# Kernel optimization log

Measured on AMD Instinct MI355X. Metric: run time of the kernel, lower is better.

The kernel has to match this reference:

```python
import jax, jax.numpy as jnp
import numpy as np

B, S, D_MODEL, N_HEADS, HEAD_DIM = 4, 2048, 1024, 16, 64
NEG = -1e9


def apply_rope_real(x, cos_f, sin_f):
    # x: [B, H, S, D]; cos_f/sin_f: [S, D//2] broadcast over B, H
    x_even = x[..., ::2]
    x_odd = x[..., 1::2]
    out_even = x_even * cos_f - x_odd * sin_f
    out_odd = x_even * sin_f + x_odd * cos_f
    return jnp.stack([out_even, out_odd], axis=-1).reshape(x.shape)


def setup_inputs() -> dict:
    key = jax.random.key(0)
    ks = jax.random.split(key, 8)
    x = jax.random.normal(ks[0], (B, S, D_MODEL), dtype=jnp.float32)
    # RoPE tables: theta_i = 10000^{-2i/d}, angles = pos * theta
    inv_freq = 1.0 / (10000.0 ** (jnp.arange(0, HEAD_DIM, 2, dtype=jnp.float32) / HEAD_DIM))
    angles = jnp.arange(S, dtype=jnp.float32)[:, None] * inv_freq[None, :]  # [S, D/2]
    cos_freqs = jnp.cos(angles)
    sin_freqs = jnp.sin(angles)
    causal_mask = jnp.where(jnp.tril(jnp.ones((S, S), dtype=bool)), 0.0, NEG).astype(jnp.float32)
    scale = 0.02
    w_q = jax.random.normal(ks[1], (D_MODEL, D_MODEL), dtype=jnp.float32) * scale
    w_k = jax.random.normal(ks[2], (D_MODEL, D_MODEL), dtype=jnp.float32) * scale
    w_v = jax.random.normal(ks[3], (D_MODEL, D_MODEL), dtype=jnp.float32) * scale
    w_o = jax.random.normal(ks[4], (D_MODEL, D_MODEL), dtype=jnp.float32) * scale
    return {"x": x, "cos_freqs": cos_freqs, "sin_freqs": sin_freqs,
            "causal_mask": causal_mask, "w_q": w_q, "w_k": w_k, "w_v": w_v, "w_o": w_o}


def reference(x, cos_freqs, sin_freqs, causal_mask, w_q, w_k, w_v, w_o):
    batch, seq_len, _ = x.shape
    scale = 1.0 / jnp.sqrt(jnp.float32(HEAD_DIM))
    # torch Linear: y = x @ W.T
    def proj(w):
        return (x @ w.T).reshape(batch, seq_len, N_HEADS, HEAD_DIM).transpose(0, 2, 1, 3)
    q = apply_rope_real(proj(w_q), cos_freqs, sin_freqs)
    k = apply_rope_real(proj(w_k), cos_freqs, sin_freqs)
    v = proj(w_v)
    attn = jnp.einsum('bhqd,bhkd->bhqk', q, k) * scale + causal_mask
    attn = jax.nn.softmax(attn, axis=-1)
    out = jnp.einsum('bhqk,bhkd->bhqd', attn, v)
    out = out.transpose(0, 2, 1, 3).reshape(batch, seq_len, -1)
    return out @ w_o.T
```

## Files before the change

kernel.cpp:

```cpp
#include <hip/hip_runtime.h>
#include <stdint.h>

#define B_  4
#define S_  2048
#define DM_ 1024
#define NH_ 16
#define HD_ 64

typedef unsigned short ushort_t;
typedef __bf16 bf16x8 __attribute__((ext_vector_type(8)));
typedef float  floatx4 __attribute__((ext_vector_type(4)));
typedef float  floatx16 __attribute__((ext_vector_type(16)));

__device__ __forceinline__ float bf2f(ushort_t u) {
    union { unsigned int i; float f; } v; v.i = ((unsigned int)u) << 16; return v.f;
}
__device__ __forceinline__ ushort_t f2bf(float f) {
    union { float f; unsigned int i; } v; v.f = f;
    unsigned int x = v.i;
    return (ushort_t)((x + 0x7fffu + ((x >> 16) & 1u)) >> 16);
}
__device__ __forceinline__ unsigned int pack_bf16_trunc(float lo, float hi) {
    union { float f; unsigned int u; } a, b;
    a.f = lo; b.f = hi;
    return __builtin_amdgcn_perm(b.u, a.u, 0x07060302u);
}

__global__ __launch_bounds__(256) void cvt_all_kernel(
    const float* __restrict__ x,  const float* __restrict__ wq,
    const float* __restrict__ wk, const float* __restrict__ wv,
    const float* __restrict__ wo,
    ushort_t* __restrict__ xb,  ushort_t* __restrict__ wqb,
    ushort_t* __restrict__ wkb, ushort_t* __restrict__ wvb,
    ushort_t* __restrict__ wob)
{
    const int blk = blockIdx.x;
    const float* src; ushort_t* dst; int off;
    if (blk < 8192)       { src = x;  dst = xb;  off = blk; }
    else if (blk < 9216)  { src = wq; dst = wqb; off = blk - 8192; }
    else if (blk < 10240) { src = wk; dst = wkb; off = blk - 9216; }
    else if (blk < 11264) { src = wv; dst = wvb; off = blk - 10240; }
    else                  { src = wo; dst = wob; off = blk - 11264; }
    const int i = off * 256 + threadIdx.x;
    float4 v = ((const float4*)src)[i];
    ushort4 o; o.x = f2bf(v.x); o.y = f2bf(v.y); o.z = f2bf(v.z); o.w = f2bf(v.w);
    ((ushort4*)dst)[i] = o;
}

__global__ __launch_bounds__(512, 2) void gemm_bt_kernel(
    const ushort_t* __restrict__ A,
    const ushort_t* __restrict__ B0, const ushort_t* __restrict__ B1,
    const ushort_t* __restrict__ B2,
    void* __restrict__ C0, void* __restrict__ C1, void* __restrict__ C2,
    int M, int N, int K, int mode, int nz)
{
    __shared__ ushort_t As[2][16384];
    __shared__ ushort_t Bs[2][8192];

    const int lid = blockIdx.x;
    const int cpx = gridDim.x >> 3;
    const int wg  = (lid & 7) * cpx + (lid >> 3);
    const int x   = wg / (8 * nz);
    const int rr  = wg - x * (8 * nz);
    const int y   = rr & 7;
    const int z   = rr >> 3;

    const ushort_t* Bw = z == 0 ? B0 : z == 1 ? B1 : B2;
    void* Cv           = z == 0 ? C0 : z == 1 ? C1 : C2;

    const int tid  = threadIdx.x;
    const int wave = tid >> 6, lane = tid & 63;
    const int l15 = lane & 15, quad = lane >> 4;
    const int wr = wave >> 1, wc = wave & 1;
    const int mbase = x * 256;
    const int nbase = y * 128;
    const int NT = K >> 6;

    auto stageA = [&](int bt, int t, int L0) {
#pragma unroll
        for (int L = L0; L < L0 + 2; ++L) {
            const int e8  = L * 512 + tid;
            const int row = e8 >> 3, c = e8 & 7;
            const ushort_t* src = A + (size_t)(mbase + row) * K + t * 64 + ((c ^ (row & 7)) << 3);
            __builtin_amdgcn_global_load_lds(
                (const __attribute__((address_space(1))) unsigned int*)src,
                (__attribute__((address_space(3))) unsigned int*)(&As[bt][e8 * 8]), 16, 0, 0);
        }
    };
    auto stageB = [&](int bt, int t, int L) {
        const int e8  = L * 512 + tid;
        const int row = e8 >> 3, c = e8 & 7;
        const ushort_t* src = Bw + (size_t)(nbase + row) * K + t * 64 + ((c ^ (row & 7)) << 3);
        __builtin_amdgcn_global_load_lds(
            (const __attribute__((address_space(1))) unsigned int*)src,
            (__attribute__((address_space(3))) unsigned int*)(&Bs[bt][e8 * 8]), 16, 0, 0);
    };

    floatx4 acc[4][4] = {};

    stageA(0, 0, 0); stageA(0, 0, 2);
    stageB(0, 0, 0); stageB(0, 0, 1);
    if (NT > 1) {
        stageB(1, 1, 0); stageB(1, 1, 1);
        asm volatile("s_waitcnt vmcnt(2)" ::: "memory");
    } else {
        asm volatile("s_waitcnt vmcnt(0)" ::: "memory");
    }
    __builtin_amdgcn_s_barrier();

    auto do_tile = [&](int t, int bt) {
        bf16x8 a0[2][2], a1[2][2], b0[2][2], b1[2][2];
#pragma unroll
        for (int kk = 0; kk < 2; ++kk) {
#pragma unroll
            for (int f = 0; f < 2; ++f) {
                const int row = wr * 64 + f * 16 + l15;
                a0[kk][f] = *(const bf16x8*)&As[bt][row * 64 + ((((kk << 2) | quad)) ^ (l15 & 7)) * 8];
            }
#pragma unroll
            for (int g = 0; g < 2; ++g) {
                const int row = wc * 64 + g * 16 + l15;
                b0[kk][g] = *(const bf16x8*)&Bs[bt][row * 64 + ((((kk << 2) | quad)) ^ (l15 & 7)) * 8];
            }
        }
        if (t + 1 < NT) stageA(bt ^ 1, t + 1, 0);
        __builtin_amdgcn_s_barrier();
        asm volatile("s_waitcnt lgkmcnt(0)" ::: "memory");
        __builtin_amdgcn_s_setprio(1);
#pragma unroll
        for (int kk = 0; kk < 2; ++kk)
#pragma unroll
            for (int mt = 0; mt < 2; ++mt)
#pragma unroll
                for (int nt = 0; nt < 2; ++nt)
                    acc[mt][nt] = __builtin_amdgcn_mfma_f32_16x16x32_bf16(
                        a0[kk][mt], b0[kk][nt], acc[mt][nt], 0, 0, 0);
        __builtin_amdgcn_s_setprio(0);
        __builtin_amdgcn_s_barrier();

#pragma unroll
        for (int kk = 0; kk < 2; ++kk)
#pragma unroll
            for (int g = 0; g < 2; ++g) {
                const int row = wc * 64 + 32 + g * 16 + l15;
                b1[kk][g] = *(const bf16x8*)&Bs[bt][row * 64 + ((((kk << 2) | quad)) ^ (l15 & 7)) * 8];
            }
        if (t + 1 < NT) stageA(bt ^ 1, t + 1, 2);
        __builtin_amdgcn_s_barrier();
        asm volatile("s_waitcnt lgkmcnt(0)" ::: "memory");
        __builtin_amdgcn_s_setprio(1);
#pragma unroll
        for (int kk = 0; kk < 2; ++kk)
#pragma unroll
            for (int mt = 0; mt < 2; ++mt)
#pragma unroll
                for (int nt = 0; nt < 2; ++nt)
                    acc[mt][2 + nt] = __builtin_amdgcn_mfma_f32_16x16x32_bf16(
                        a0[kk][mt], b1[kk][nt], acc[mt][2 + nt], 0, 0, 0);
        __builtin_amdgcn_s_setprio(0);
        __builtin_amdgcn_s_barrier();

#pragma unroll
        for (int kk = 0; kk < 2; ++kk)
#pragma unroll
            for (int f = 0; f < 2; ++f) {
                const int row = wr * 64 + 32 + f * 16 + l15;
                a1[kk][f] = *(const bf16x8*)&As[bt][row * 64 + ((((kk << 2) | quad)) ^ (l15 & 7)) * 8];
            }
        if (t + 2 < NT) stageB(bt, t + 2, 0);
        __builtin_amdgcn_s_barrier();
        asm volatile("s_waitcnt lgkmcnt(0)" ::: "memory");
        __builtin_amdgcn_s_setprio(1);
#pragma unroll
        for (int kk = 0; kk < 2; ++kk)
#pragma unroll
            for (int mt = 0; mt < 2; ++mt)
#pragma unroll
                for (int nt = 0; nt < 2; ++nt)
                    acc[2 + mt][2 + nt] = __builtin_amdgcn_mfma_f32_16x16x32_bf16(
                        a1[kk][mt], b1[kk][nt], acc[2 + mt][2 + nt], 0, 0, 0);
        __builtin_amdgcn_s_setprio(0);
        __builtin_amdgcn_s_barrier();

        if (t + 2 < NT) stageB(bt, t + 2, 1);
        __builtin_amdgcn_s_barrier();
        __builtin_amdgcn_s_setprio(1);
#pragma unroll
        for (int kk = 0; kk < 2; ++kk)
#pragma unroll
            for (int mt = 0; mt < 2; ++mt)
#pragma unroll
                for (int nt = 0; nt < 2; ++nt)
                    acc[2 + mt][nt] = __builtin_amdgcn_mfma_f32_16x16x32_bf16(
                        a1[kk][mt], b0[kk][nt], acc[2 + mt][nt], 0, 0, 0);
        __builtin_amdgcn_s_setprio(0);
        if (t + 2 < NT) { asm volatile("s_waitcnt vmcnt(2)" ::: "memory"); }
        else            { asm volatile("s_waitcnt vmcnt(0)" ::: "memory"); }
        __builtin_amdgcn_s_barrier();
    };

    for (int t = 0; t < NT; t += 2) {
        do_tile(t, 0);
        do_tile(t + 1, 1);
    }

    const bool vtmode = (mode == 0) && (z == 2);
#pragma unroll
    for (int mt = 0; mt < 4; ++mt) {
#pragma unroll
        for (int nt = 0; nt < 4; ++nt) {
            const int col = nbase + wc * 64 + nt * 16 + l15;
            const int m0  = mbase + wr * 64 + mt * 16 + quad * 4;
            if (vtmode) {
                const int b = m0 >> 11, s = m0 & 2047;
                const int hh = col >> 6, d = col & 63;
                uint2 pk;
                pk.x = (unsigned)f2bf(acc[mt][nt][0]) | ((unsigned)f2bf(acc[mt][nt][1]) << 16);
                pk.y = (unsigned)f2bf(acc[mt][nt][2]) | ((unsigned)f2bf(acc[mt][nt][3]) << 16);
                *(uint2*)&((ushort_t*)Cv)[((size_t)((b * NH_ + hh) * HD_ + d)) * S_ + s] = pk;
            } else if (mode == 0) {
#pragma unroll
                for (int r = 0; r < 4; ++r) {
                    const int m = m0 + r;
                    const int b = m >> 11, s = m & 2047;
                    const int hh = col >> 6, d = col & 63;
                    ((ushort_t*)Cv)[(((size_t)(b * NH_ + hh)) * S_ + s) * HD_ + d] =
                        f2bf(acc[mt][nt][r]);
                }
            } else {
#pragma unroll
                for (int r = 0; r < 4; ++r)
                    ((float*)Cv)[(size_t)(m0 + r) * N + col] = acc[mt][nt][r];
            }
        }
    }
}

#define QSCALE 0.1803368801f
__global__ __launch_bounds__(256) void rope_kernel(
    ushort_t* __restrict__ q, ushort_t* __restrict__ k,
    const float* __restrict__ cf, const float* __restrict__ sf)
{
    const int idx = blockIdx.x * 256 + threadIdx.x;
    const int j = idx & 31;
    const int s = (idx >> 5) & (S_ - 1);
    const float c  = cf[s * 32 + j];
    const float sn = sf[s * 32 + j];
    const size_t base = (size_t)idx * 2;
    float qe = bf2f(q[base]), qo = bf2f(q[base + 1]);
    q[base]     = f2bf((qe * c - qo * sn) * QSCALE);
    q[base + 1] = f2bf((qe * sn + qo * c) * QSCALE);
    float ke = bf2f(k[base]), ko = bf2f(k[base + 1]);
    k[base]     = f2bf(ke * c - ko * sn);
    k[base + 1] = f2bf(ke * sn + ko * c);
}

__global__ __launch_bounds__(256, 2) void attn_kernel(
    const ushort_t* __restrict__ Qg, const ushort_t* __restrict__ Kg,
    const ushort_t* __restrict__ Vg, ushort_t* __restrict__ Og)
{
    __shared__ ushort_t Ks[2][64 * 64];
    __shared__ ushort_t Vt[2][64 * 64];
    __shared__ ushort_t Pt[4][32 * 64];

    const int pair = blockIdx.x;
    const int bh   = blockIdx.y;
    const int tid  = threadIdx.x;
    const int wave = tid >> 6, lane = tid & 63;
    const int l31 = lane & 31, h = lane >> 5;

    const size_t bh_off = (size_t)bh * S_ * HD_;
    const int pswz = (l31 & 7) << 3;
    const int b_out = bh >> 4, h_out = bh & 15;

    const int e0 = tid, e1 = tid + 256;
    const int r0 = e0 >> 3, c0 = (e0 & 7) ^ (r0 & 7);
    const int r1 = e1 >> 3, c1 = (e1 & 7) ^ (r1 & 7);

#pragma unroll 1
    for (int seg = 0; seg < 2; ++seg) {
        const int qtile = seg ? (15 - pair) : pair;
        const int qbase = qtile * 128;
        const int nkt   = 2 * qtile + 2;
        const int qrow  = qbase + wave * 32 + l31;

        bf16x8 qf[4];
#pragma unroll
        for (int ks = 0; ks < 4; ++ks)
            qf[ks] = *(const bf16x8*)(Qg + bh_off + (size_t)qrow * HD_ + ks * 16 + h * 8);

        float m_run = -1e30f, l_run = 0.f;
        floatx16 o_acc[2] = {};

        {
            const ushort_t* ka = Kg + bh_off + (size_t)r0 * HD_ + c0 * 8;
            const ushort_t* kb = Kg + bh_off + (size_t)r1 * HD_ + c1 * 8;
            const ushort_t* va = Vg + bh_off + (size_t)r0 * S_ + c0 * 8;
            const ushort_t* vb = Vg + bh_off + (size_t)r1 * S_ + c1 * 8;
            __builtin_amdgcn_global_load_lds(
                (const __attribute__((address_space(1))) unsigned int*)ka,
                (__attribute__((address_space(3))) unsigned int*)(&Ks[0][e0 * 8]), 16, 0, 0);
            __builtin_amdgcn_global_load_lds(
                (const __attribute__((address_space(1))) unsigned int*)kb,
                (__attribute__((address_space(3))) unsigned int*)(&Ks[0][e1 * 8]), 16, 0, 0);
            __builtin_amdgcn_global_load_lds(
                (const __attribute__((address_space(1))) unsigned int*)va,
                (__attribute__((address_space(3))) unsigned int*)(&Vt[0][e0 * 8]), 16, 0, 0);
            __builtin_amdgcn_global_load_lds(
                (const __attribute__((address_space(1))) unsigned int*)vb,
                (__attribute__((address_space(3))) unsigned int*)(&Vt[0][e1 * 8]), 16, 0, 0);
        }
        asm volatile("s_waitcnt vmcnt(0)" ::: "memory");
        __syncthreads();

        for (int kt = 0; kt < nkt; ++kt) {
            const int kbase = kt * 64;
            const int cur = kt & 1;

            if (kt + 1 < nkt) {
                const int nb = kbase + 64;
                const ushort_t* ka = Kg + bh_off + (size_t)(nb + r0) * HD_ + c0 * 8;
                const ushort_t* kb = Kg + bh_off + (size_t)(nb + r1) * HD_ + c1 * 8;
                const ushort_t* va = Vg + bh_off + (size_t)r0 * S_ + nb + c0 * 8;
                const ushort_t* vb = Vg + bh_off + (size_t)r1 * S_ + nb + c1 * 8;
                __builtin_amdgcn_global_load_lds(
                    (const __attribute__((address_space(1))) unsigned int*)ka,
                    (__attribute__((address_space(3))) unsigned int*)(&Ks[cur ^ 1][e0 * 8]), 16, 0, 0);
                __builtin_amdgcn_global_load_lds(
                    (const __attribute__((address_space(1))) unsigned int*)kb,
                    (__attribute__((address_space(3))) unsigned int*)(&Ks[cur ^ 1][e1 * 8]), 16, 0, 0);
                __builtin_amdgcn_global_load_lds(
                    (const __attribute__((address_space(1))) unsigned int*)va,
                    (__attribute__((address_space(3))) unsigned int*)(&Vt[cur ^ 1][e0 * 8]), 16, 0, 0);
                __builtin_amdgcn_global_load_lds(
                    (const __attribute__((address_space(1))) unsigned int*)vb,
                    (__attribute__((address_space(3))) unsigned int*)(&Vt[cur ^ 1][e1 * 8]), 16, 0, 0);
            }

            if (kbase <= qbase + wave * 32 + 31) {
                floatx16 st[2] = {};
#pragma unroll
                for (int nt = 0; nt < 2; ++nt) {
                    const int krow = nt * 32 + l31;
#pragma unroll
                    for (int ks = 0; ks < 4; ++ks) {
                        bf16x8 kf = *(const bf16x8*)&Ks[cur][krow * 64 +
                                        (((ks * 2 + h) ^ (l31 & 7)) << 3)];
                        st[nt] = __builtin_amdgcn_mfma_f32_32x32x16_bf16(kf, qf[ks], st[nt], 0, 0, 0);
                    }
                }
                if (kbase + 63 > qbase + wave * 32) {
#pragma unroll
                    for (int nt = 0; nt < 2; ++nt) {
                        const int key0 = kbase + nt * 32 + 4 * h;
#pragma unroll
                        for (int c = 0; c < 4; ++c)
#pragma unroll
                            for (int r = 0; r < 4; ++r)
                                if (key0 + 8 * c + r > qrow) st[nt][c * 4 + r] = -1e9f;
                    }
                }
                float mx = st[0][0];
#pragma unroll
                for (int nt = 0; nt < 2; ++nt)
#pragma unroll
                    for (int i = 0; i < 16; ++i) mx = fmaxf(mx, st[nt][i]);
                mx = fmaxf(mx, __shfl_xor(mx, 32, 64));
                const float mnew = fmaxf(m_run, mx);
                const float alpha = __builtin_amdgcn_exp2f(m_run - mnew);
                m_run = mnew;
                float sum = 0.f;
#pragma unroll
                for (int nt = 0; nt < 2; ++nt)
#pragma unroll
                    for (int i = 0; i < 16; ++i) {
                        const float p = __builtin_amdgcn_exp2f(st[nt][i] - mnew);
                        st[nt][i] = p; sum += p;
                    }
                sum += __shfl_xor(sum, 32, 64);
                l_run = l_run * alpha + sum;
#pragma unroll
                for (int dt = 0; dt < 2; ++dt)
#pragma unroll
                    for (int i = 0; i < 16; ++i) o_acc[dt][i] *= alpha;

                ushort_t* pr = &Pt[wave][l31 * 64];
#pragma unroll
                for (int nt = 0; nt < 2; ++nt)
#pragma unroll
                    for (int c = 0; c < 4; ++c) {
                        uint2 pk;
                        pk.x = pack_bf16_trunc(st[nt][c * 4 + 0], st[nt][c * 4 + 1]);
                        pk.y = pack_bf16_trunc(st[nt][c * 4 + 2], st[nt][c * 4 + 3]);
                        *(uint2*)(pr + (((nt * 32 + 8 * c) ^ pswz) + 4 * h)) = pk;
                    }
                __builtin_amdgcn_fence(__ATOMIC_ACQ_REL, "wavefront");
                __builtin_amdgcn_wave_barrier();

                bf16x8 pf[4];
#pragma unroll
                for (int ks = 0; ks < 4; ++ks)
                    pf[ks] = *(const bf16x8*)(&Pt[wave][l31 * 64 + ((ks * 16 + h * 8) ^ pswz)]);

#pragma unroll
                for (int dt = 0; dt < 2; ++dt) {
                    const int d = dt * 32 + l31;
#pragma unroll
                    for (int ks = 0; ks < 4; ++ks) {
                        bf16x8 vf = *(const bf16x8*)&Vt[cur][d * 64 +
                                        (((ks * 2 + h) ^ (l31 & 7)) << 3)];
                        o_acc[dt] = __builtin_amdgcn_mfma_f32_32x32x16_bf16(vf, pf[ks], o_acc[dt], 0, 0, 0);
                    }
                }
            }

            asm volatile("s_waitcnt vmcnt(0)" ::: "memory");
            __syncthreads();
        }

        const float inv = 1.0f / l_run;
        ushort_t* orow = Og + ((size_t)(b_out * S_ + qrow)) * DM_ + h_out * HD_;
#pragma unroll
        for (int dt = 0; dt < 2; ++dt)
#pragma unroll
            for (int c = 0; c < 4; ++c) {
                uint2 pk;
                pk.x = (unsigned)f2bf(o_acc[dt][c * 4 + 0] * inv) |
                       ((unsigned)f2bf(o_acc[dt][c * 4 + 1] * inv) << 16);
                pk.y = (unsigned)f2bf(o_acc[dt][c * 4 + 2] * inv) |
                       ((unsigned)f2bf(o_acc[dt][c * 4 + 3] * inv) << 16);
                *(uint2*)(orow + dt * 32 + 8 * c + 4 * h) = pk;
            }
    }
}

extern "C" void kernel_launch(void* const* d_in, const int* in_sizes, int n_in,
                              void* d_out, int out_size, void* d_ws, size_t ws_size,
                              hipStream_t stream)
{
    const float* x  = (const float*)d_in[0];
    const float* cf = (const float*)d_in[1];
    const float* sf = (const float*)d_in[2];
    const float* wq = (const float*)d_in[4];
    const float* wk = (const float*)d_in[5];
    const float* wv = (const float*)d_in[6];
    const float* wo = (const float*)d_in[7];
    float* out = (float*)d_out;

    const size_t NELEM = (size_t)B_ * S_ * DM_;
    const size_t WELEM = (size_t)DM_ * DM_;
    ushort_t* xb  = (ushort_t*)d_ws;
    ushort_t* qb  = xb + NELEM;
    ushort_t* kb  = qb + NELEM;
    ushort_t* vb  = kb + NELEM;
    ushort_t* ao  = vb + NELEM;
    ushort_t* wqb = ao + NELEM;
    ushort_t* wkb = wqb + WELEM;
    ushort_t* wvb = wkb + WELEM;
    ushort_t* wob = wvb + WELEM;

    cvt_all_kernel<<<dim3(8192 + 4 * 1024), 256, 0, stream>>>(
        x, wq, wk, wv, wo, xb, wqb, wkb, wvb, wob);

    const int M = B_ * S_;
    gemm_bt_kernel<<<dim3(32 * 8 * 3), 512, 0, stream>>>(
        xb, wqb, wkb, wvb, qb, kb, vb, M, DM_, DM_, 0, 3);
    rope_kernel<<<dim3((B_ * NH_ * S_ * 32) / 256), 256, 0, stream>>>(qb, kb, cf, sf);
    attn_kernel<<<dim3(8, B_ * NH_), 256, 0, stream>>>(qb, kb, vb, ao);
    gemm_bt_kernel<<<dim3(32 * 8), 512, 0, stream>>>(
        ao, wob, wob, wob, out, out, out, M, DM_, DM_, 1, 1);
}
```

Baseline: 285.8 us.

## Rework attention scheduling, keep P in registers via permlane swap, lazy rescale

Each attention block now handles a single q-tile instead of a pair, with 1024 blocks ordered longest-first and batch-heads interleaved across the grid. Occupancy rises to four blocks per CU. The P matrix is no longer staged through LDS; it is repacked in registers with permlane32_swap, which removes the Pt buffer and a wave barrier. Online-softmax rescaling is skipped unless the running max grows by more than a threshold, trading some exp range headroom for fewer multiplies.

```diff
diff --git a/kernel.cpp b/kernel.cpp
--- a/kernel.cpp
+++ b/kernel.cpp
@@ -255,183 +255,185 @@
     k[base + 1] = f2bf(ke * sn + ko * c);
 }
 
-__global__ __launch_bounds__(256, 2) void attn_kernel(
+__global__ __launch_bounds__(256, 4) void attn_kernel(
     const ushort_t* __restrict__ Qg, const ushort_t* __restrict__ Kg,
     const ushort_t* __restrict__ Vg, ushort_t* __restrict__ Og)
 {
     __shared__ ushort_t Ks[2][64 * 64];
     __shared__ ushort_t Vt[2][64 * 64];
-    __shared__ ushort_t Pt[4][32 * 64];
-
-    const int pair = blockIdx.x;
-    const int bh   = blockIdx.y;
+
+    const int id   = blockIdx.x;
+    const int sg   = id >> 3;
+    const int bh   = (id & 7) * 8 + (sg & 7);
+    const int qtile = 15 - (sg >> 3);
     const int tid  = threadIdx.x;
     const int wave = tid >> 6, lane = tid & 63;
     const int l31 = lane & 31, h = lane >> 5;
 
     const size_t bh_off = (size_t)bh * S_ * HD_;
-    const int pswz = (l31 & 7) << 3;
     const int b_out = bh >> 4, h_out = bh & 15;
 
     const int e0 = tid, e1 = tid + 256;
     const int r0 = e0 >> 3, c0 = (e0 & 7) ^ (r0 & 7);
     const int r1 = e1 >> 3, c1 = (e1 & 7) ^ (r1 & 7);
 
-#pragma unroll 1
-    for (int seg = 0; seg < 2; ++seg) {
-        const int qtile = seg ? (15 - pair) : pair;
-        const int qbase = qtile * 128;
-        const int nkt   = 2 * qtile + 2;
-        const int qrow  = qbase + wave * 32 + l31;
-
-        bf16x8 qf[4];
-#pragma unroll
-        for (int ks = 0; ks < 4; ++ks)
-            qf[ks] = *(const bf16x8*)(Qg + bh_off + (size_t)qrow * HD_ + ks * 16 + h * 8);
-
-        float m_run = -1e30f, l_run = 0.f;
-        floatx16 o_acc[2] = {};
-
-        {
-            const ushort_t* ka = Kg + bh_off + (size_t)r0 * HD_ + c0 * 8;
-            const ushort_t* kb = Kg + bh_off + (size_t)r1 * HD_ + c1 * 8;
-            const ushort_t* va = Vg + bh_off + (size_t)r0 * S_ + c0 * 8;
-            const ushort_t* vb = Vg + bh_off + (size_t)r1 * S_ + c1 * 8;
+    const int qbase = qtile * 128;
+    const int nkt   = 2 * qtile + 2;
+    const int qrow  = qbase + wave * 32 + l31;
+
+    bf16x8 qf[4];
+#pragma unroll
+    for (int ks = 0; ks < 4; ++ks)
+        qf[ks] = *(const bf16x8*)(Qg + bh_off + (size_t)qrow * HD_ + ks * 16 + h * 8);
+
+    float m_run = -1e30f, l_run = 0.f;
+    floatx16 o_acc[2] = {};
+
+    {
+        const ushort_t* ka = Kg + bh_off + (size_t)r0 * HD_ + c0 * 8;
+        const ushort_t* kb = Kg + bh_off + (size_t)r1 * HD_ + c1 * 8;
+        const ushort_t* va = Vg + bh_off + (size_t)r0 * S_ + c0 * 8;
+        const ushort_t* vb = Vg + bh_off + (size_t)r1 * S_ + c1 * 8;
+        __builtin_amdgcn_global_load_lds(
+            (const __attribute__((address_space(1))) unsigned int*)ka,
+            (__attribute__((address_space(3))) unsigned int*)(&Ks[0][e0 * 8]), 16, 0, 0);
+        __builtin_amdgcn_global_load_lds(
+            (const __attribute__((address_space(1))) unsigned int*)kb,
+            (__attribute__((address_space(3))) unsigned int*)(&Ks[0][e1 * 8]), 16, 0, 0);
+        __builtin_amdgcn_global_load_lds(
+            (const __attribute__((address_space(1))) unsigned int*)va,
+            (__attribute__((address_space(3))) unsigned int*)(&Vt[0][e0 * 8]), 16, 0, 0);
+        __builtin_amdgcn_global_load_lds(
+            (const __attribute__((address_space(1))) unsigned int*)vb,
+            (__attribute__((address_space(3))) unsigned int*)(&Vt[0][e1 * 8]), 16, 0, 0);
+    }
+    asm volatile("s_waitcnt vmcnt(0)" ::: "memory");
+    __syncthreads();
+
+    for (int kt = 0; kt < nkt; ++kt) {
+        const int kbase = kt * 64;
+        const int cur = kt & 1;
+
+        if (kt + 1 < nkt) {
+            const int nb = kbase + 64;
+            const ushort_t* ka = Kg + bh_off + (size_t)(nb + r0) * HD_ + c0 * 8;
+            const ushort_t* kb = Kg + bh_off + (size_t)(nb + r1) * HD_ + c1 * 8;
+            const ushort_t* va = Vg + bh_off + (size_t)r0 * S_ + nb + c0 * 8;
+            const ushort_t* vb = Vg + bh_off + (size_t)r1 * S_ + nb + c1 * 8;
             __builtin_amdgcn_global_load_lds(
                 (const __attribute__((address_space(1))) unsigned int*)ka,
-                (__attribute__((address_space(3))) unsigned int*)(&Ks[0][e0 * 8]), 16, 0, 0);
+                (__attribute__((address_space(3))) unsigned int*)(&Ks[cur ^ 1][e0 * 8]), 16, 0, 0);
             __builtin_amdgcn_global_load_lds(
                 (const __attribute__((address_space(1))) unsigned int*)kb,
-                (__attribute__((address_space(3))) unsigned int*)(&Ks[0][e1 * 8]), 16, 0, 0);
+                (__attribute__((address_space(3))) unsigned int*)(&Ks[cur ^ 1][e1 * 8]), 16, 0, 0);
             __builtin_amdgcn_global_load_lds(
                 (const __attribute__((address_space(1))) unsigned int*)va,
-                (__attribute__((address_space(3))) unsigned int*)(&Vt[0][e0 * 8]), 16, 0, 0);
+                (__attribute__((address_space(3))) unsigned int*)(&Vt[cur ^ 1][e0 * 8]), 16, 0, 0);
             __builtin_amdgcn_global_load_lds(
                 (const __attribute__((address_space(1))) unsigned int*)vb,
-                (__attribute__((address_space(3))) unsigned int*)(&Vt[0][e1 * 8]), 16, 0, 0);
-        }
-        asm volatile("s_waitcnt vmcnt(0)" ::: "memory");
-        __syncthreads();
-
-        for (int kt = 0; kt < nkt; ++kt) {
-            const int kbase = kt * 64;
-            const int cur = kt & 1;
-
-            if (kt + 1 < nkt) {
-                const int nb = kbase + 64;
-                const ushort_t* ka = Kg + bh_off + (size_t)(nb + r0) * HD_ + c0 * 8;
-                const ushort_t* kb = Kg + bh_off + (size_t)(nb + r1) * HD_ + c1 * 8;
-                const ushort_t* va = Vg + bh_off + (size_t)r0 * S_ + nb + c0 * 8;
-                const ushort_t* vb = Vg + bh_off + (size_t)r1 * S_ + nb + c1 * 8;
-                __builtin_amdgcn_global_load_lds(
-                    (const __attribute__((address_space(1))) unsigned int*)ka,
-                    (__attribute__((address_space(3))) unsigned int*)(&Ks[cur ^ 1][e0 * 8]), 16, 0, 0);
-                __builtin_amdgcn_global_load_lds(
-                    (const __attribute__((address_space(1))) unsigned int*)kb,
-                    (__attribute__((address_space(3))) unsigned int*)(&Ks[cur ^ 1][e1 * 8]), 16, 0, 0);
-                __builtin_amdgcn_global_load_lds(
-                    (const __attribute__((address_space(1))) unsigned int*)va,
-                    (__attribute__((address_space(3))) unsigned int*)(&Vt[cur ^ 1][e0 * 8]), 16, 0, 0);
-                __builtin_amdgcn_global_load_lds(
-                    (const __attribute__((address_space(1))) unsigned int*)vb,
-                    (__attribute__((address_space(3))) unsigned int*)(&Vt[cur ^ 1][e1 * 8]), 16, 0, 0);
-            }
-
-            if (kbase <= qbase + wave * 32 + 31) {
-                floatx16 st[2] = {};
+                (__attribute__((address_space(3))) unsigned int*)(&Vt[cur ^ 1][e1 * 8]), 16, 0, 0);
+        }
+
+        if (kbase <= qbase + wave * 32 + 31) {
+            floatx16 st[2] = {};
+#pragma unroll
+            for (int nt = 0; nt < 2; ++nt) {
+                const int krow = nt * 32 + l31;
+#pragma unroll
+                for (int ks = 0; ks < 4; ++ks) {
+                    bf16x8 kf = *(const bf16x8*)&Ks[cur][krow * 64 +
+                                    (((ks * 2 + h) ^ (l31 & 7)) << 3)];
+                    st[nt] = __builtin_amdgcn_mfma_f32_32x32x16_bf16(kf, qf[ks], st[nt], 0, 0, 0);
+                }
+            }
+            if (kbase + 63 > qbase + wave * 32) {
 #pragma unroll
                 for (int nt = 0; nt < 2; ++nt) {
-                    const int krow = nt * 32 + l31;
-#pragma unroll
-                    for (int ks = 0; ks < 4; ++ks) {
-                        bf16x8 kf = *(const bf16x8*)&Ks[cur][krow * 64 +
-                                        (((ks * 2 + h) ^ (l31 & 7)) << 3)];
-                        st[nt] = __builtin_amdgcn_mfma_f32_32x32x16_bf16(kf, qf[ks], st[nt], 0, 0, 0);
-                    }
-                }
-                if (kbase + 63 > qbase + wave * 32) {
-#pragma unroll
-                    for (int nt = 0; nt < 2; ++nt) {
-                        const int key0 = kbase + nt * 32 + 4 * h;
-#pragma unroll
-                        for (int c = 0; c < 4; ++c)
-#pragma unroll
-                            for (int r = 0; r < 4; ++r)
-                                if (key0 + 8 * c + r > qrow) st[nt][c * 4 + r] = -1e9f;
-                    }
-                }
-                float mx = st[0][0];
-#pragma unroll
-                for (int nt = 0; nt < 2; ++nt)
-#pragma unroll
-                    for (int i = 0; i < 16; ++i) mx = fmaxf(mx, st[nt][i]);
-                mx = fmaxf(mx, __shfl_xor(mx, 32, 64));
+                    const int key0 = kbase + nt * 32 + 4 * h;
+#pragma unroll
+                    for (int c = 0; c < 4; ++c)
+#pragma unroll
+                        for (int r = 0; r < 4; ++r)
+                            if (key0 + 8 * c + r > qrow) st[nt][c * 4 + r] = -1e9f;
+                }
+            }
+            float mx = st[0][0];
+#pragma unroll
+            for (int nt = 0; nt < 2; ++nt)
+#pragma unroll
+                for (int i = 0; i < 16; ++i) mx = fmaxf(mx, st[nt][i]);
+            mx = fmaxf(mx, __shfl_xor(mx, 32, 64));
+            if (!__all(mx <= m_run + 8.0f)) {
                 const float mnew = fmaxf(m_run, mx);
                 const float alpha = __builtin_amdgcn_exp2f(m_run - mnew);
                 m_run = mnew;
-                float sum = 0.f;
-#pragma unroll
-                for (int nt = 0; nt < 2; ++nt)
-#pragma unroll
-                    for (int i = 0; i < 16; ++i) {
-                        const float p = __builtin_amdgcn_exp2f(st[nt][i] - mnew);
-                        st[nt][i] = p; sum += p;
-                    }
-                sum += __shfl_xor(sum, 32, 64);
-                l_run = l_run * alpha + sum;
+                l_run *= alpha;
 #pragma unroll
                 for (int dt = 0; dt < 2; ++dt)
 #pragma unroll
                     for (int i = 0; i < 16; ++i) o_acc[dt][i] *= alpha;
-
-                ushort_t* pr = &Pt[wave][l31 * 64];
-#pragma unroll
-                for (int nt = 0; nt < 2; ++nt)
-#pragma unroll
-                    for (int c = 0; c < 4; ++c) {
-                        uint2 pk;
-                        pk.x = pack_bf16_trunc(st[nt][c * 4 + 0], st[nt][c * 4 + 1]);
-                        pk.y = pack_bf16_trunc(st[nt][c * 4 + 2], st[nt][c * 4 + 3]);
-                        *(uint2*)(pr + (((nt * 32 + 8 * c) ^ pswz) + 4 * h)) = pk;
-                    }
-                __builtin_amdgcn_fence(__ATOMIC_ACQ_REL, "wavefront");
-                __builtin_amdgcn_wave_barrier();
-
-                bf16x8 pf[4];
-#pragma unroll
-                for (int ks = 0; ks < 4; ++ks)
-                    pf[ks] = *(const bf16x8*)(&Pt[wave][l31 * 64 + ((ks * 16 + h * 8) ^ pswz)]);
-
-#pragma unroll
-                for (int dt = 0; dt < 2; ++dt) {
-                    const int d = dt * 32 + l31;
-#pragma unroll
-                    for (int ks = 0; ks < 4; ++ks) {
-                        bf16x8 vf = *(const bf16x8*)&Vt[cur][d * 64 +
-                                        (((ks * 2 + h) ^ (l31 & 7)) << 3)];
-                        o_acc[dt] = __builtin_amdgcn_mfma_f32_32x32x16_bf16(vf, pf[ks], o_acc[dt], 0, 0, 0);
-                    }
-                }
-            }
-
-            asm volatile("s_waitcnt vmcnt(0)" ::: "memory");
-            __syncthreads();
-        }
-
-        const float inv = 1.0f / l_run;
-        ushort_t* orow = Og + ((size_t)(b_out * S_ + qrow)) * DM_ + h_out * HD_;
-#pragma unroll
-        for (int dt = 0; dt < 2; ++dt)
-#pragma unroll
-            for (int c = 0; c < 4; ++c) {
-                uint2 pk;
-                pk.x = (unsigned)f2bf(o_acc[dt][c * 4 + 0] * inv) |
-                       ((unsigned)f2bf(o_acc[dt][c * 4 + 1] * inv) << 16);
-                pk.y = (unsigned)f2bf(o_acc[dt][c * 4 + 2] * inv) |
-                       ((unsigned)f2bf(o_acc[dt][c * 4 + 3] * inv) << 16);
-                *(uint2*)(orow + dt * 32 + 8 * c + 4 * h) = pk;
-            }
+            }
+            float sum = 0.f;
+#pragma unroll
+            for (int nt = 0; nt < 2; ++nt)
+#pragma unroll
+                for (int i = 0; i < 16; ++i) {
+                    const float p = __builtin_amdgcn_exp2f(st[nt][i] - m_run);
+                    st[nt][i] = p; sum += p;
+                }
+            sum += __shfl_xor(sum, 32, 64);
+            l_run += sum;
+
+            bf16x8 pf[4];
+#pragma unroll
+            for (int ks = 0; ks < 4; ++ks) {
+                const int nt = ks >> 1, base = (ks & 1) * 8;
+                unsigned wrd[4];
+#pragma unroll
+                for (int d8 = 0; d8 < 2; ++d8) {
+                    unsigned p = pack_bf16_trunc(st[nt][base + 2 * d8],
+                                                 st[nt][base + 2 * d8 + 1]);
+                    unsigned q = pack_bf16_trunc(st[nt][base + 4 + 2 * d8],
+                                                 st[nt][base + 4 + 2 * d8 + 1]);
+                    auto r = __builtin_amdgcn_permlane32_swap((int)p, (int)q, false, false);
+                    wrd[d8]     = (unsigned)r[0];
+                    wrd[2 + d8] = (unsigned)r[1];
+                }
+                union { unsigned u[4]; bf16x8 v; } cvt;
+                cvt.u[0] = wrd[0]; cvt.u[1] = wrd[1];
+                cvt.u[2] = wrd[2]; cvt.u[3] = wrd[3];
+                pf[ks] = cvt.v;
+            }
+
+#pragma unroll
+            for (int dt = 0; dt < 2; ++dt) {
+                const int d = dt * 32 + l31;
+#pragma unroll
+                for (int ks = 0; ks < 4; ++ks) {
+                    bf16x8 vf = *(const bf16x8*)&Vt[cur][d * 64 +
+                                    (((ks * 2 + h) ^ (l31 & 7)) << 3)];
+                    o_acc[dt] = __builtin_amdgcn_mfma_f32_32x32x16_bf16(vf, pf[ks], o_acc[dt], 0, 0, 0);
+                }
+            }
+        }
+
+        asm volatile("s_waitcnt vmcnt(0)" ::: "memory");
+        __syncthreads();
     }
+
+    const float inv = 1.0f / l_run;
+    ushort_t* orow = Og + ((size_t)(b_out * S_ + qrow)) * DM_ + h_out * HD_;
+#pragma unroll
+    for (int dt = 0; dt < 2; ++dt)
+#pragma unroll
+        for (int c = 0; c < 4; ++c) {
+            uint2 pk;
+            pk.x = (unsigned)f2bf(o_acc[dt][c * 4 + 0] * inv) |
+                   ((unsigned)f2bf(o_acc[dt][c * 4 + 1] * inv) << 16);
+            pk.y = (unsigned)f2bf(o_acc[dt][c * 4 + 2] * inv) |
+                   ((unsigned)f2bf(o_acc[dt][c * 4 + 3] * inv) << 16);
+            *(uint2*)(orow + dt * 32 + 8 * c + 4 * h) = pk;
+        }
 }
 
 extern "C" void kernel_launch(void* const* d_in, const int* in_sizes, int n_in,
@@ -466,7 +468,7 @@
     gemm_bt_kernel<<<dim3(32 * 8 * 3), 512, 0, stream>>>(
         xb, wqb, wkb, wvb, qb, kb, vb, M, DM_, DM_, 0, 3);
     rope_kernel<<<dim3((B_ * NH_ * S_ * 32) / 256), 256, 0, stream>>>(qb, kb, cf, sf);
-    attn_kernel<<<dim3(8, B_ * NH_), 256, 0, stream>>>(qb, kb, vb, ao);
+    attn_kernel<<<dim3(1024), 256, 0, stream>>>(qb, kb, vb, ao);
     gemm_bt_kernel<<<dim3(32 * 8), 512, 0, stream>>>(
         ao, wob, wob, wob, out, out, out, M, DM_, DM_, 1, 1);
 }
```

Result: faster. 272.1 us (-4.8%).
